# Performance work log

Measured on AMD Instinct MI355X. Metric: run time of the kernel, lower is better.

## Reference

```python
import jax, jax.numpy as jnp
import numpy as np

L1, L2, L3, L4 = 0.01, 0.001, 0.1, 100.0
DROP_P = 0.3

def setup_inputs() -> dict:
    key = jax.random.key(0)
    ks = jax.random.split(key, 6)
    n, p, h, c = 262144, 256, 256, 10
    x = jax.random.normal(ks[0], (n, p), dtype=jnp.float32)
    y = jax.random.randint(ks[1], (n,), 0, c, dtype=jnp.int64)
    drop_u = jax.random.uniform(ks[2], (n, h), dtype=jnp.float32)
    b1 = jax.random.normal(ks[3], (p, h), dtype=jnp.float32) / p
    b2 = jax.random.normal(ks[4], (h, c), dtype=jnp.float32) / h
    w = jax.random.normal(ks[5], (n, 1), dtype=jnp.float32) / n + 1.0 / np.sqrt(n).astype(np.float32)
    return {"x": x, "y": y, "drop_u": drop_u, "b1": b1, "b2": b2, "w": w}

def reference(x, y, drop_u, b1, b2, w):
    n, p = x.shape
    # MLP: ReLU -> Dropout(0.3) (inverted dropout, deterministic mask from drop_u)
    hdn = jax.nn.relu(x @ b1)
    keep = (drop_u > DROP_P).astype(x.dtype) / (1.0 - DROP_P)
    logits = (hdn * keep) @ b2  # [n, 10]
    pred = jnp.argmax(logits, axis=1)
    weight = w * w  # [n, 1]
    # per-sample CE; torch broadcast ce[n] * weight[n,1] -> [n,n], summed == ce.sum()*weight.sum()
    ce = -jnp.take_along_axis(jax.nn.log_softmax(logits, axis=-1), y[:, None], axis=1)[:, 0]
    loss = ce.sum() * weight.sum()
    # balancing regularizer: x.T @ diag(weight) @ x computed as column-scale-then-GEMM
    col = x.T @ weight  # [p, 1]
    gram = x.T @ (weight * x)  # [p, p] == x.T @ diag(weight) @ x
    bm = (gram - col @ col.T) * (1.0 - jnp.eye(p, dtype=x.dtype))
    loss = loss + L1 * (jnp.abs(b1).sum() + jnp.abs(b2).sum())
    loss = loss + L2 * jnp.sum(bm * bm)
    loss = loss + L3 * jnp.sum(weight * weight)
    loss = loss + L4 * (weight.sum() - 1.0) ** 2
    acc = jnp.mean((pred == y).astype(jnp.float32))
    return (loss, acc)
```

## Files before the change

### kernel.cpp

```cpp
#include <hip/hip_runtime.h>
#include <hip/hip_bf16.h>
#include <math.h>

typedef __bf16 v8bf  __attribute__((ext_vector_type(8)));
typedef __bf16 v4bf  __attribute__((ext_vector_type(4)));
typedef float  v16f  __attribute__((ext_vector_type(16)));
typedef float  v4f   __attribute__((ext_vector_type(4)));
typedef float  f4v   __attribute__((ext_vector_type(4)));

#define OFF_COL   16
#define OFF_GRAM  1024
#define OFF_WT    263168
#define B1T_BYTE  2101248
#define B2T_BYTE  2232320
#define ZERO_BYTES 1052672

extern "C" __global__ __launch_bounds__(256) void prep_k(
    const float* __restrict__ w, const float* __restrict__ b1,
    const float* __restrict__ b2, float* __restrict__ wsf) {
  float* weight = wsf + OFF_WT;
  __bf16* b1T = (__bf16*)((char*)wsf + B1T_BYTE);
  __bf16* b2T = (__bf16*)((char*)wsf + B2T_BYTE);
  int gid = blockIdx.x * 256 + threadIdx.x;
  float wi = w[gid];
  float wt = wi * wi;
  weight[gid] = wt;
  float s1 = wt, s2 = wt * wt, a1 = 0.f, a2 = 0.f;
  if (gid < 65536) {
    int h = gid >> 8, p = gid & 255;
    float v = b1[p * 256 + h];
    b1T[gid] = (__bf16)v;
    a1 = fabsf(v);
  }
  if (gid < 4096) {
    int c = gid >> 8, h = gid & 255;
    float v = (c < 10) ? b2[h * 10 + c] : 0.f;
    b2T[gid] = (__bf16)v;
    a2 = fabsf(v);
  }
  #pragma unroll
  for (int off = 32; off > 0; off >>= 1) {
    s1 += __shfl_down(s1, off);
    s2 += __shfl_down(s2, off);
    a1 += __shfl_down(a1, off);
    a2 += __shfl_down(a2, off);
  }
  if ((threadIdx.x & 63) == 0) {
    atomicAdd(&wsf[1], s1);
    atomicAdd(&wsf[2], s2);
    if (blockIdx.x < 256) atomicAdd(&wsf[3], a1);
    if (blockIdx.x < 16)  atomicAdd(&wsf[4], a2);
  }
}

extern "C" __global__ __launch_bounds__(512, 2) void gram_k(
    const float* __restrict__ x, float* __restrict__ wsf) {
  const float* weight = wsf + OFF_WT;
  float* gram = wsf + OFF_GRAM + (blockIdx.x & 3) * 65536;
  __shared__ __bf16 xT[256 * 72];
  __shared__ __bf16 wxT[256 * 72];
  const int tid = threadIdx.x;
  const int wv = tid >> 6, L = tid & 63;
  const int l32 = L & 31, lh = L >> 5;
  const int mb = 64 * (wv >> 1), nb = 128 * (wv & 1);
  const int col = tid & 255, rh = tid >> 8;
  const int base = blockIdx.x * 1024;
  v16f acc[2][4] = {};
  float colAcc = 0.f;

  for (int ch = 0; ch < 16; ch++) {
    int k0 = base + 64 * ch;
    __syncthreads();
    #pragma unroll
    for (int s = 0; s < 8; s++) {
      int krow = 32 * rh + 4 * s;
      float v0 = x[(k0 + krow + 0) * 256 + col];
      float v1 = x[(k0 + krow + 1) * 256 + col];
      float v2 = x[(k0 + krow + 2) * 256 + col];
      float v3 = x[(k0 + krow + 3) * 256 + col];
      float w0 = weight[k0 + krow + 0];
      float w1 = weight[k0 + krow + 1];
      float w2 = weight[k0 + krow + 2];
      float w3 = weight[k0 + krow + 3];
      colAcc += w0 * v0 + w1 * v1 + w2 * v2 + w3 * v3;
      v4bf xa, wa;
      xa[0] = (__bf16)v0; xa[1] = (__bf16)v1; xa[2] = (__bf16)v2; xa[3] = (__bf16)v3;
      wa[0] = (__bf16)(w0 * v0); wa[1] = (__bf16)(w1 * v1);
      wa[2] = (__bf16)(w2 * v2); wa[3] = (__bf16)(w3 * v3);
      *(v4bf*)&xT[col * 72 + krow]  = xa;
      *(v4bf*)&wxT[col * 72 + krow] = wa;
    }
    __syncthreads();
    #pragma unroll
    for (int ks = 0; ks < 64; ks += 16) {
      v8bf a0 = *(const v8bf*)&xT[(mb + l32) * 72 + ks + 8 * lh];
      v8bf a1 = *(const v8bf*)&xT[(mb + 32 + l32) * 72 + ks + 8 * lh];
      v8bf b[4];
      #pragma unroll
      for (int tn = 0; tn < 4; tn++)
        b[tn] = *(const v8bf*)&wxT[(nb + 32 * tn + l32) * 72 + ks + 8 * lh];
      #pragma unroll
      for (int tn = 0; tn < 4; tn++) {
        acc[0][tn] = __builtin_amdgcn_mfma_f32_32x32x16_bf16(a0, b[tn], acc[0][tn], 0, 0, 0);
        acc[1][tn] = __builtin_amdgcn_mfma_f32_32x32x16_bf16(a1, b[tn], acc[1][tn], 0, 0, 0);
      }
    }
  }
  #pragma unroll
  for (int tm = 0; tm < 2; tm++)
    #pragma unroll
    for (int tn = 0; tn < 4; tn++)
      #pragma unroll
      for (int r = 0; r < 16; r++) {
        int row = mb + 32 * tm + (r & 3) + 8 * (r >> 2) + 4 * lh;
        int cg = nb + 32 * tn + l32;
        atomicAdd(&gram[row * 256 + cg], acc[tm][tn][r]);
      }
  atomicAdd(&wsf[OFF_COL + col], colAcc);
}

extern "C" __global__ __launch_bounds__(256, 4) void mlp_k(
    const float* __restrict__ x, const int* __restrict__ y,
    const float* __restrict__ du, float* __restrict__ wsf) {
  const __bf16* b1T = (const __bf16*)((const char*)wsf + B1T_BYTE);
  const __bf16* b2T = (const __bf16*)((const char*)wsf + B2T_BYTE);
  __shared__ union U {
    struct { __bf16 xs[64 * 40]; __bf16 b1s[256 * 40]; } m;
    struct { __bf16 hk[64 * 264]; float lg[64 * 16]; } l;
  } sm;
  const int tid = threadIdx.x;
  const int wv = tid >> 6, L = tid & 63;
  const int l32 = L & 31, lh = L >> 5;
  const int nb = 64 * wv;
  const int rowBase = blockIdx.x * 64;

  v16f acc[2][2] = {};

  for (int kc = 0; kc < 256; kc += 32) {
    __syncthreads();
    #pragma unroll
    for (int i = 0; i < 2; i++) {
      int f = tid + 256 * i;
      int r = f >> 3, c4 = f & 7;
      f4v v = ((const f4v*)x)[(rowBase + r) * 64 + (kc >> 2) + c4];
      v4bf o;
      o[0] = (__bf16)v[0]; o[1] = (__bf16)v[1]; o[2] = (__bf16)v[2]; o[3] = (__bf16)v[3];
      *(v4bf*)&sm.m.xs[r * 40 + 4 * c4] = o;
    }
    #pragma unroll
    for (int i = 0; i < 4; i++) {
      int f = tid + 256 * i;
      int nr = f >> 2, c = f & 3;
      *(v8bf*)&sm.m.b1s[nr * 40 + 8 * c] = *(const v8bf*)&b1T[nr * 256 + kc + 8 * c];
    }
    __syncthreads();
    #pragma unroll
    for (int ks = 0; ks < 32; ks += 16) {
      v8bf a0 = *(const v8bf*)&sm.m.xs[(l32) * 40 + ks + 8 * lh];
      v8bf a1 = *(const v8bf*)&sm.m.xs[(32 + l32) * 40 + ks + 8 * lh];
      v8bf b0 = *(const v8bf*)&sm.m.b1s[(nb + l32) * 40 + ks + 8 * lh];
      v8bf b1f = *(const v8bf*)&sm.m.b1s[(nb + 32 + l32) * 40 + ks + 8 * lh];
      acc[0][0] = __builtin_amdgcn_mfma_f32_32x32x16_bf16(a0, b0,  acc[0][0], 0, 0, 0);
      acc[0][1] = __builtin_amdgcn_mfma_f32_32x32x16_bf16(a0, b1f, acc[0][1], 0, 0, 0);
      acc[1][0] = __builtin_amdgcn_mfma_f32_32x32x16_bf16(a1, b0,  acc[1][0], 0, 0, 0);
      acc[1][1] = __builtin_amdgcn_mfma_f32_32x32x16_bf16(a1, b1f, acc[1][1], 0, 0, 0);
    }
  }
  #pragma unroll
  for (int tm = 0; tm < 2; tm++)
    #pragma unroll
    for (int tn = 0; tn < 2; tn++)
      #pragma unroll
      for (int r = 0; r < 16; r++) {
        int row = 32 * tm + (r & 3) + 8 * (r >> 2) + 4 * lh;
        int cg = nb + 32 * tn + l32;
        float u = du[(rowBase + row) * 256 + cg];
        float v = acc[tm][tn][r];
        v = fmaxf(v, 0.f);
        acc[tm][tn][r] = (u > 0.3f) ? v * (1.0f / 0.7f) : 0.f;
      }

  __syncthreads();
  #pragma unroll
  for (int tm = 0; tm < 2; tm++)
    #pragma unroll
    for (int tn = 0; tn < 2; tn++)
      #pragma unroll
      for (int r = 0; r < 16; r++) {
        int row = 32 * tm + (r & 3) + 8 * (r >> 2) + 4 * lh;
        int cg = nb + 32 * tn + l32;
        sm.l.hk[row * 264 + cg] = (__bf16)acc[tm][tn][r];
      }
  __syncthreads();
  v4f lacc = {};
  #pragma unroll
  for (int kk = 0; kk < 8; kk++) {
    v8bf a  = *(const v8bf*)&sm.l.hk[(16 * wv + (L & 15)) * 264 + 32 * kk + 8 * (L >> 4)];
    v8bf bb = *(const v8bf*)&b2T[(L & 15) * 256 + 32 * kk + 8 * (L >> 4)];
    lacc = __builtin_amdgcn_mfma_f32_16x16x32_bf16(a, bb, lacc, 0, 0, 0);
  }
  #pragma unroll
  for (int r = 0; r < 4; r++)
    sm.l.lg[(16 * wv + 4 * (L >> 4) + r) * 16 + (L & 15)] = lacc[r];
  __syncthreads();
  float ce = 0.f;
  int cor = 0;
  if (tid < 64) {
    const float* lr = &sm.l.lg[tid * 16];
    float mx = lr[0];
    int am = 0;
    #pragma unroll
    for (int c = 1; c < 10; c++)
      if (lr[c] > mx) { mx = lr[c]; am = c; }
    float s = 0.f;
    #pragma unroll
    for (int c = 0; c < 10; c++) s += expf(lr[c] - mx);
    int yt = y[rowBase + tid];
    ce = logf(s) + mx - lr[yt];
    cor = (am == yt) ? 1 : 0;
  }
  if (wv == 0) {
    #pragma unroll
    for (int off = 32; off > 0; off >>= 1) ce += __shfl_down(ce, off);
    unsigned long long bal = __ballot(cor != 0);
    if (L == 0) {
      atomicAdd(&wsf[0], ce);
      atomicAdd((int*)&wsf[8], (int)__popcll(bal));
    }
  }
}

extern "C" __global__ __launch_bounds__(1024) void fin_k(
    const float* __restrict__ wsf, float* __restrict__ out) {
  __shared__ float colS[256];
  __shared__ float red[1024];
  int tid = threadIdx.x;
  if (tid < 256) colS[tid] = wsf[OFF_COL + tid];
  __syncthreads();
  int t = tid & 255, q = tid >> 8;
  const float* g = wsf + OFF_GRAM;
  float ct = colS[t];
  float bm = 0.f;
  for (int j = 64 * q; j < 64 * q + 64; j++) {
    float gv = g[j * 256 + t] + g[65536 + j * 256 + t]
             + g[131072 + j * 256 + t] + g[196608 + j * 256 + t];
    float d = gv - colS[j] * ct;
    bm += (j != t) ? d * d : 0.f;
  }
  red[tid] = bm;
  __syncthreads();
  for (int s = 512; s > 0; s >>= 1) {
    if (tid < s) red[tid] += red[tid + s];
    __syncthreads();
  }
  if (tid == 0) {
    float ce = wsf[0], wsum = wsf[1], w4 = wsf[2], ab1 = wsf[3], ab2 = wsf[4];
    int cor = *(const int*)&wsf[8];
    float loss = ce * wsum
               + 0.01f * (ab1 + ab2)
               + 0.001f * red[0]
               + 0.1f * w4
               + 100.f * (wsum - 1.f) * (wsum - 1.f);
    out[0] = loss;
    out[1] = (float)cor * (1.0f / 262144.0f);
  }
}

extern "C" void kernel_launch(void* const* d_in, const int* in_sizes, int n_in,
                              void* d_out, int out_size, void* d_ws, size_t ws_size,
                              hipStream_t stream) {
  const float* x  = (const float*)d_in[0];
  const int*   y  = (const int*)d_in[1];
  const float* du = (const float*)d_in[2];
  const float* b1 = (const float*)d_in[3];
  const float* b2 = (const float*)d_in[4];
  const float* w  = (const float*)d_in[5];
  float* wsf = (float*)d_ws;

  hipMemsetAsync(d_ws, 0, ZERO_BYTES, stream);
  prep_k<<<1024, 256, 0, stream>>>(w, b1, b2, wsf);
  gram_k<<<256, 512, 0, stream>>>(x, wsf);
  mlp_k<<<4096, 256, 0, stream>>>(x, y, du, wsf);
  fin_k<<<1, 1024, 0, stream>>>(wsf, (float*)d_out);
}
```

Measured before the change: 820.3 us.

## Double-buffer gram tiles and replace atomic gram reduction with per-block slots

The gram kernel now prefetches the next 64-row chunk of x into registers while MFMAs run on the current LDS buffer, using double-buffered LDS and a shared-memory copy of the weights. Each block writes its partial gram to its own 256KB slot instead of doing float atomics into four shared copies. A new 256-block gfin_k reduces the slots and computes the balancing term in parallel, replacing the single-block fin_k loop. The slots add 64MB of extra writes and reads of workspace and one more launch, and the double buffers raise LDS use and register pressure, which can lower occupancy.

```diff
diff --git a/kernel.cpp b/kernel.cpp
--- a/kernel.cpp
+++ b/kernel.cpp
@@ -9,11 +9,11 @@
 typedef float  f4v   __attribute__((ext_vector_type(4)));
 
 #define OFF_COL   16
-#define OFF_GRAM  1024
-#define OFF_WT    263168
-#define B1T_BYTE  2101248
-#define B2T_BYTE  2232320
-#define ZERO_BYTES 1052672
+#define OFF_WT    512
+#define OFF_SLOT  262656
+#define B1T_BYTE  68159488
+#define B2T_BYTE  68290560
+#define ZERO_BYTES 1088
 
 extern "C" __global__ __launch_bounds__(256) void prep_k(
     const float* __restrict__ w, const float* __restrict__ b1,
@@ -56,9 +56,10 @@
 extern "C" __global__ __launch_bounds__(512, 2) void gram_k(
     const float* __restrict__ x, float* __restrict__ wsf) {
   const float* weight = wsf + OFF_WT;
-  float* gram = wsf + OFF_GRAM + (blockIdx.x & 3) * 65536;
-  __shared__ __bf16 xT[256 * 72];
-  __shared__ __bf16 wxT[256 * 72];
+  float* slot = wsf + OFF_SLOT + blockIdx.x * 65536;
+  __shared__ __bf16 xT[2][256 * 72];
+  __shared__ __bf16 wxT[2][256 * 72];
+  __shared__ float  wS[1024];
   const int tid = threadIdx.x;
   const int wv = tid >> 6, L = tid & 63;
   const int l32 = L & 31, lh = L >> 5;
@@ -67,45 +68,75 @@
   const int base = blockIdx.x * 1024;
   v16f acc[2][4] = {};
   float colAcc = 0.f;
+  float xv[32];
+
+  wS[tid] = weight[base + tid];
+  wS[tid + 512] = weight[base + 512 + tid];
+
+  #pragma unroll
+  for (int j = 0; j < 32; j++)
+    xv[j] = x[(base + 32 * rh + j) * 256 + col];
+  __syncthreads();
+  #pragma unroll
+  for (int s = 0; s < 8; s++) {
+    v4bf xa, wa;
+    #pragma unroll
+    for (int i = 0; i < 4; i++) {
+      int kr = 32 * rh + 4 * s + i;
+      float v = xv[4 * s + i];
+      float wvv = wS[kr] * v;
+      colAcc += wvv;
+      xa[i] = (__bf16)v;
+      wa[i] = (__bf16)wvv;
+    }
+    *(v4bf*)&xT[0][col * 72 + 32 * rh + 4 * s]  = xa;
+    *(v4bf*)&wxT[0][col * 72 + 32 * rh + 4 * s] = wa;
+  }
+  __syncthreads();
 
   for (int ch = 0; ch < 16; ch++) {
-    int k0 = base + 64 * ch;
-    __syncthreads();
-    #pragma unroll
-    for (int s = 0; s < 8; s++) {
-      int krow = 32 * rh + 4 * s;
-      float v0 = x[(k0 + krow + 0) * 256 + col];
-      float v1 = x[(k0 + krow + 1) * 256 + col];
-      float v2 = x[(k0 + krow + 2) * 256 + col];
-      float v3 = x[(k0 + krow + 3) * 256 + col];
-      float w0 = weight[k0 + krow + 0];
-      float w1 = weight[k0 + krow + 1];
-      float w2 = weight[k0 + krow + 2];
-      float w3 = weight[k0 + krow + 3];
-      colAcc += w0 * v0 + w1 * v1 + w2 * v2 + w3 * v3;
-      v4bf xa, wa;
-      xa[0] = (__bf16)v0; xa[1] = (__bf16)v1; xa[2] = (__bf16)v2; xa[3] = (__bf16)v3;
-      wa[0] = (__bf16)(w0 * v0); wa[1] = (__bf16)(w1 * v1);
-      wa[2] = (__bf16)(w2 * v2); wa[3] = (__bf16)(w3 * v3);
-      *(v4bf*)&xT[col * 72 + krow]  = xa;
-      *(v4bf*)&wxT[col * 72 + krow] = wa;
-    }
-    __syncthreads();
+    const int cur = ch & 1, nxt = cur ^ 1;
+    if (ch < 15) {
+      int k0 = base + 64 * (ch + 1);
+      #pragma unroll
+      for (int j = 0; j < 32; j++)
+        xv[j] = x[(k0 + 32 * rh + j) * 256 + col];
+    }
     #pragma unroll
     for (int ks = 0; ks < 64; ks += 16) {
-      v8bf a0 = *(const v8bf*)&xT[(mb + l32) * 72 + ks + 8 * lh];
-      v8bf a1 = *(const v8bf*)&xT[(mb + 32 + l32) * 72 + ks + 8 * lh];
+      v8bf a0 = *(const v8bf*)&xT[cur][(mb + l32) * 72 + ks + 8 * lh];
+      v8bf a1 = *(const v8bf*)&xT[cur][(mb + 32 + l32) * 72 + ks + 8 * lh];
       v8bf b[4];
       #pragma unroll
       for (int tn = 0; tn < 4; tn++)
-        b[tn] = *(const v8bf*)&wxT[(nb + 32 * tn + l32) * 72 + ks + 8 * lh];
+        b[tn] = *(const v8bf*)&wxT[cur][(nb + 32 * tn + l32) * 72 + ks + 8 * lh];
       #pragma unroll
       for (int tn = 0; tn < 4; tn++) {
         acc[0][tn] = __builtin_amdgcn_mfma_f32_32x32x16_bf16(a0, b[tn], acc[0][tn], 0, 0, 0);
         acc[1][tn] = __builtin_amdgcn_mfma_f32_32x32x16_bf16(a1, b[tn], acc[1][tn], 0, 0, 0);
       }
     }
-  }
+    if (ch < 15) {
+      const int wb = 64 * (ch + 1);
+      #pragma unroll
+      for (int s = 0; s < 8; s++) {
+        v4bf xa, wa;
+        #pragma unroll
+        for (int i = 0; i < 4; i++) {
+          int kr = 32 * rh + 4 * s + i;
+          float v = xv[4 * s + i];
+          float wvv = wS[wb + kr] * v;
+          colAcc += wvv;
+          xa[i] = (__bf16)v;
+          wa[i] = (__bf16)wvv;
+        }
+        *(v4bf*)&xT[nxt][col * 72 + 32 * rh + 4 * s]  = xa;
+        *(v4bf*)&wxT[nxt][col * 72 + 32 * rh + 4 * s] = wa;
+      }
+      __syncthreads();
+    }
+  }
+
   #pragma unroll
   for (int tm = 0; tm < 2; tm++)
     #pragma unroll
@@ -114,9 +145,31 @@
       for (int r = 0; r < 16; r++) {
         int row = mb + 32 * tm + (r & 3) + 8 * (r >> 2) + 4 * lh;
         int cg = nb + 32 * tn + l32;
-        atomicAdd(&gram[row * 256 + cg], acc[tm][tn][r]);
+        slot[row * 256 + cg] = acc[tm][tn][r];
       }
   atomicAdd(&wsf[OFF_COL + col], colAcc);
+}
+
+extern "C" __global__ __launch_bounds__(256) void gfin_k(float* __restrict__ wsf) {
+  __shared__ float partial[4][256];
+  const int tid = threadIdx.x;
+  const int sg = tid >> 6, l = tid & 63;
+  const int row = blockIdx.x;
+  const float* slot0 = wsf + OFF_SLOT;
+  f4v s = {0.f, 0.f, 0.f, 0.f};
+  #pragma unroll 4
+  for (int sl = sg; sl < 256; sl += 4)
+    s += ((const f4v*)(slot0 + sl * 65536 + row * 256))[l];
+  *(f4v*)&partial[sg][4 * l] = s;
+  __syncthreads();
+  float cr = wsf[OFF_COL + row];
+  float ct = wsf[OFF_COL + tid];
+  float gv = partial[0][tid] + partial[1][tid] + partial[2][tid] + partial[3][tid];
+  float d = gv - cr * ct;
+  float bm = (tid != row) ? d * d : 0.f;
+  #pragma unroll
+  for (int off = 32; off > 0; off >>= 1) bm += __shfl_down(bm, off);
+  if (l == 0) atomicAdd(&wsf[5], bm);
 }
 
 extern "C" __global__ __launch_bounds__(256, 4) void mlp_k(
@@ -230,35 +283,13 @@
   }
 }
 
-extern "C" __global__ __launch_bounds__(1024) void fin_k(
-    const float* __restrict__ wsf, float* __restrict__ out) {
-  __shared__ float colS[256];
-  __shared__ float red[1024];
-  int tid = threadIdx.x;
-  if (tid < 256) colS[tid] = wsf[OFF_COL + tid];
-  __syncthreads();
-  int t = tid & 255, q = tid >> 8;
-  const float* g = wsf + OFF_GRAM;
-  float ct = colS[t];
-  float bm = 0.f;
-  for (int j = 64 * q; j < 64 * q + 64; j++) {
-    float gv = g[j * 256 + t] + g[65536 + j * 256 + t]
-             + g[131072 + j * 256 + t] + g[196608 + j * 256 + t];
-    float d = gv - colS[j] * ct;
-    bm += (j != t) ? d * d : 0.f;
-  }
-  red[tid] = bm;
-  __syncthreads();
-  for (int s = 512; s > 0; s >>= 1) {
-    if (tid < s) red[tid] += red[tid + s];
-    __syncthreads();
-  }
-  if (tid == 0) {
-    float ce = wsf[0], wsum = wsf[1], w4 = wsf[2], ab1 = wsf[3], ab2 = wsf[4];
-    int cor = *(const int*)&wsf[8];
+extern "C" __global__ void fin2_k(const float* __restrict__ wsf, float* __restrict__ out) {
+  if (threadIdx.x == 0) {
+    float ce = wsf[0], wsum = wsf[1], w4 = wsf[2], ab1 = wsf[3], ab2 = wsf[4], bm = wsf[5];
+    int cor = ((const int*)wsf)[8];
     float loss = ce * wsum
                + 0.01f * (ab1 + ab2)
-               + 0.001f * red[0]
+               + 0.001f * bm
                + 0.1f * w4
                + 100.f * (wsum - 1.f) * (wsum - 1.f);
     out[0] = loss;
@@ -280,6 +311,7 @@
   hipMemsetAsync(d_ws, 0, ZERO_BYTES, stream);
   prep_k<<<1024, 256, 0, stream>>>(w, b1, b2, wsf);
   gram_k<<<256, 512, 0, stream>>>(x, wsf);
+  gfin_k<<<256, 256, 0, stream>>>(wsf);
   mlp_k<<<4096, 256, 0, stream>>>(x, y, du, wsf);
-  fin_k<<<1, 1024, 0, stream>>>(wsf, (float*)d_out);
-}
+  fin2_k<<<1, 64, 0, stream>>>(wsf, (float*)d_out);
+}
```

Result: faster. 769.2 us (-6.2%).
